# Kernel tuning notes

Measured on AMD Instinct MI355X. Metric: run time of the kernel, lower is better.

Reference implementation:

```python
import jax, jax.numpy as jnp
import numpy as np

K = 9          # kernel points along H (morph=0 -> kernel shape (9,1))
PAD = K // 2   # same padding along H
EPS = 1e-5     # batchnorm eps


def setup_inputs() -> dict:
    key = jax.random.key(0)
    ks = jax.random.split(key, 6)
    B, Cin, Cout, H, W = 4, 64, 64, 160, 160
    x = jax.random.normal(ks[0], (B, Cin, H, W), jnp.float32)
    # offset branch conv: 2*K offset channels, kernel (K,1)
    w_off = jax.random.normal(ks[1], (2 * K, Cin, K, 1), jnp.float32) * 0.05
    b_off = jax.random.normal(ks[2], (2 * K,), jnp.float32) * 0.05
    gamma = jnp.ones((2 * K,), jnp.float32)
    beta = jnp.zeros((2 * K,), jnp.float32)
    # deformable conv weights: kernel (K,1), groups=1
    w_def = jax.random.normal(ks[3], (Cout, Cin, K, 1), jnp.float32) * 0.05
    b_def = jax.random.normal(ks[4], (Cout,), jnp.float32) * 0.05
    return {"x": x, "w_off": w_off, "b_off": b_off, "gamma": gamma,
            "beta": beta, "w_def": w_def, "b_def": b_def}


def _convert_offsets(off):
    # morph=0: even channels (x) -> 0; odd channels (y) -> per-kernel-point cumsum
    c = K // 2
    y = off[:, 1::2]                                            # [B,K,H,W]
    top = jnp.flip(jnp.cumsum(jnp.flip(y[:, :c + 1], 1), 1), 1)  # suffix-cumsum to center
    bot = jnp.cumsum(jnp.concatenate([top[:, c:c + 1], y[:, c + 1:]], 1), 1)
    y_new = jnp.concatenate([top[:, :c], bot], 1)
    return jnp.zeros_like(off).at[:, 1::2].set(y_new)


def _deform_conv(x, off, w, b):
    B, C, H, W = x.shape
    dy = off[:, 0::2]                                           # [B,K,H,W]
    dx = off[:, 1::2]
    ky = jnp.arange(K, dtype=x.dtype).reshape(1, K, 1, 1)
    py = jnp.arange(H, dtype=x.dtype).reshape(1, 1, H, 1) - PAD + ky + dy
    px = jnp.arange(W, dtype=x.dtype).reshape(1, 1, 1, W) + dx
    y0 = jnp.floor(py)
    x0 = jnp.floor(px)
    fy = py - y0
    fx = px - x0
    y0i = y0.astype(jnp.int32)
    x0i = x0.astype(jnp.int32)
    xf = x.reshape(B, C, H * W)

    def gather(yc, xc):
        # zero-padded bilinear corner gather -> [B,C,K,H,W]
        valid = ((yc >= 0) & (yc < H) & (xc >= 0) & (xc < W)).astype(x.dtype)
        lin = jnp.clip(yc, 0, H - 1) * W + jnp.clip(xc, 0, W - 1)
        v = jax.vmap(lambda img, idx: img[:, idx])(xf, lin)
        return v * valid[:, None]

    w00 = ((1 - fy) * (1 - fx))[:, None]
    w01 = ((1 - fy) * fx)[:, None]
    w10 = (fy * (1 - fx))[:, None]
    w11 = (fy * fx)[:, None]
    samples = (w00 * gather(y0i, x0i) + w01 * gather(y0i, x0i + 1)
               + w10 * gather(y0i + 1, x0i) + w11 * gather(y0i + 1, x0i + 1))
    # contract kernel points and input channels
    return jnp.einsum('bckhw,ock->bohw', samples, w[:, :, :, 0]) + b[None, :, None, None]


def reference(x, w_off, b_off, gamma, beta, w_def, b_def):
    # offset branch: conv -> batchnorm (training-mode stats) -> tanh -> snake cumsum
    off = jax.lax.conv_general_dilated(
        x, w_off, (1, 1), ((PAD, PAD), (0, 0)),
        dimension_numbers=('NCHW', 'OIHW', 'NCHW')) + b_off[None, :, None, None]
    mu = off.mean((0, 2, 3), keepdims=True)
    var = off.var((0, 2, 3), keepdims=True)
    off = (off - mu) * jax.lax.rsqrt(var + EPS) * gamma[None, :, None, None] + beta[None, :, None, None]
    off = _convert_offsets(jnp.tanh(off))
    return _deform_conv(x, off, w_def, b_def)
```

## Files before the change

### kernel.cpp

```cpp
#include <hip/hip_runtime.h>
#include <hip/hip_fp16.h>
#include <math.h>

#define HW    25600
#define WID   160
#define HEI   160
#define BB    4
#define CIN   64
#define COUT  64
#define NBN   102400
#define TSTR  162

typedef _Float16 f16x8 __attribute__((ext_vector_type(8)));
typedef float    f32x4 __attribute__((ext_vector_type(4)));

union U4 { int i[4]; f16x8 v; };
union HU { unsigned u; __half2 h; };

__device__ __forceinline__ unsigned short f2h(float f) {
    return __half_as_ushort(__float2half(f));
}

__device__ __forceinline__ float ftanh(float x) {
    float e = __builtin_amdgcn_exp2f(x * 2.8853900817779268f);
    return 1.0f - 2.0f * __builtin_amdgcn_rcpf(e + 1.0f);
}

__global__ __launch_bounds__(256) void p0_prep(
        const float* __restrict__ x, const float* __restrict__ w_def,
        const float* __restrict__ w_off,
        unsigned short* __restrict__ xbT, unsigned short* __restrict__ wtA,
        unsigned short* __restrict__ wofA, float* __restrict__ stats) {
    int t = threadIdx.x;
    int blk = blockIdx.x;
    if (blk == 640) {
        for (int u = 0; u < 144; ++u) {
            int idx = t + u * 256;
            int k = idx >> 12;
            int r = idx & 4095;
            int chalf = r >> 11;
            int og = (r >> 9) & 3;
            int L = (r >> 3) & 63;
            int j = idx & 7;
            int o = og * 16 + (L & 15);
            int c = chalf * 32 + (L >> 4) * 8 + j;
            wtA[idx] = f2h(w_def[(o * CIN + c) * 9 + k]);
        }
        for (int u = 0; u < 36; ++u) {
            int idx = t + u * 256;
            int jj = idx & 7;
            int L  = (idx >> 3) & 63;
            int ch = (idx >> 9) & 1;
            int k  = idx >> 10;
            int j  = L & 15;
            int c  = ch * 32 + (L >> 4) * 8 + jj;
            wofA[idx] = (j < 9) ? f2h(w_off[((2 * j + 1) * CIN + c) * 9 + k])
                                : (unsigned short)0;
        }
        if (t < 32) stats[t] = 0.f;
        return;
    }
    __shared__ __align__(16) unsigned short tile[CIN * TSTR];
    int b = blk / HEI, h = blk % HEI;
    const float* xp = x + (b * CIN) * HW + h * WID;
    unsigned* ti = (unsigned*)tile;
#pragma unroll
    for (int u = 0; u < 10; ++u) {
        int e = t + u * 256;
        int c = e / 40, wq = e - c * 40;
        const float4 v = *(const float4*)(xp + c * HW + 4 * wq);
        unsigned p01 = f2h(v.x) | ((unsigned)f2h(v.y) << 16);
        unsigned p23 = f2h(v.z) | ((unsigned)f2h(v.w) << 16);
        ti[81 * c + 2 * wq]     = p01;
        ti[81 * c + 2 * wq + 1] = p23;
    }
    __syncthreads();
    unsigned* dst = (unsigned*)(xbT + (b * HEI + h) * (WID * 64));
#pragma unroll
    for (int u = 0; u < 20; ++u) {
        int e = t + u * 256;
        int w = e >> 5, cp = e & 31;
        unsigned lo = tile[(2 * cp) * TSTR + w];
        unsigned hi = tile[(2 * cp + 1) * TSTR + w];
        dst[e] = lo | (hi << 16);
    }
}

__global__ __launch_bounds__(320) void k1_offconv_mfma(
        const unsigned short* __restrict__ xbT,
        const unsigned short* __restrict__ wofA,
        const float* __restrict__ b_off,
        float* __restrict__ off_odd, float* __restrict__ stats) {
    int t = threadIdx.x;
    int blk = blockIdx.x;
    int xcd = blk & 7;
    int idx = blk >> 3;
    int b   = idx / 40;
    int r2  = idx - b * 40;
    int h   = xcd * 20 + (r2 >> 1);
    int p0  = (r2 & 1) * 80;
    int wave = t >> 6, lane = t & 63;
    int l15 = lane & 15, q = lane >> 4;
    int px  = p0 + wave * 16 + l15;

    f32x4 acc = (f32x4){0.f, 0.f, 0.f, 0.f};

    int klo = 4 - h;   if (klo < 0) klo = 0;
    int khi = 163 - h; if (khi > 8) khi = 8;

    for (int k = klo; k <= khi; ++k) {
        int py = h + k - 4;
        const unsigned short* sp = xbT + (b * HEI + py) * (WID * 64) + px * 64;
        f16x8 a0 = *(const f16x8*)(wofA + ((k * 2 + 0) * 64 + lane) * 8);
        f16x8 a1 = *(const f16x8*)(wofA + ((k * 2 + 1) * 64 + lane) * 8);
        f16x8 b0 = *(const f16x8*)(sp + q * 8);
        f16x8 b1 = *(const f16x8*)(sp + 32 + q * 8);
        acc = __builtin_amdgcn_mfma_f32_16x16x32_f16(a0, b0, acc, 0, 0, 0);
        acc = __builtin_amdgcn_mfma_f32_16x16x32_f16(a1, b1, acc, 0, 0, 0);
    }

    float sS[4] = {0.f, 0.f, 0.f, 0.f}, sQ[4] = {0.f, 0.f, 0.f, 0.f};
#pragma unroll
    for (int r = 0; r < 4; ++r) {
        int j = q * 4 + r;
        if (j < 9) {
            float v = acc[r] + b_off[2 * j + 1];
            off_odd[(b * 9 + j) * HW + h * WID + px] = v;
            sS[r] = v; sQ[r] = v * v;
        }
    }
#pragma unroll
    for (int o = 1; o < 16; o <<= 1) {
#pragma unroll
        for (int r = 0; r < 4; ++r) {
            sS[r] += __shfl_xor(sS[r], o);
            sQ[r] += __shfl_xor(sQ[r], o);
        }
    }
    __shared__ float redS[5][16], redQ[5][16];
    if (l15 == 0) {
#pragma unroll
        for (int r = 0; r < 4; ++r) {
            int j = q * 4 + r;
            if (j < 9) { redS[wave][j] = sS[r]; redQ[wave][j] = sQ[r]; }
        }
    }
    __syncthreads();
    if (t < 18) {
        int j = (t < 9) ? t : t - 9;
        float v = 0.f;
#pragma unroll
        for (int w = 0; w < 5; ++w)
            v += (t < 9) ? redS[w][j] : redQ[w][j];
        atomicAdd(&stats[t], v);
    }
}

__global__ __launch_bounds__(256, 5) void k4_deform_mfma(
        const unsigned short* __restrict__ xbT,
        const float* __restrict__ off_odd,
        const float* __restrict__ stats,
        const float* __restrict__ gamma,
        const float* __restrict__ beta,
        const unsigned short* __restrict__ wtA,
        const float* __restrict__ b_def,
        float* __restrict__ out) {
    __shared__ __align__(16) int S[2][80 * 36];
    __shared__ unsigned P0h[9][80], P1h[9][80];
    __shared__ int      PXI[9][80];

    int t   = threadIdx.x;
    int blk = blockIdx.x;
    int xcd = blk & 7;
    int idx = blk >> 3;
    int b   = idx / 40;
    int r2  = idx - b * 40;
    int h   = xcd * 20 + (r2 >> 1);
    int p0  = (r2 & 1) * 80;
    int wave = t >> 6, lane = t & 63;
    int l15 = lane & 15, q = lane >> 4;

    if (t < 80) {
        int px = p0 + t;
        float tv[9];
#pragma unroll
        for (int j = 0; j < 9; ++j) {
            float mean = stats[j] * (1.0f / NBN);
            float var  = stats[9 + j] * (1.0f / NBN) - mean * mean;
            float inv  = rsqrtf(var + 1e-5f);
            float v = off_odd[(b * 9 + j) * HW + h * WID + px];
            tv[j] = ftanh((v - mean) * inv * gamma[2 * j + 1] + beta[2 * j + 1]);
        }
        float dxv[9];
        dxv[4] = tv[4];
#pragma unroll
        for (int i = 5; i < 9; ++i) dxv[i] = dxv[i - 1] + tv[i];
#pragma unroll
        for (int i = 3; i >= 0; --i) dxv[i] = dxv[i + 1] + tv[i];
#pragma unroll
        for (int j = 0; j < 9; ++j) {
            int py = h + j - 4;
            bool rowok = (py >= 0) && (py < HEI);
            float pxf = (float)px + dxv[j];
            float x0f = floorf(pxf);
            float fx  = pxf - x0f;
            int   x0  = (int)x0f;
            float s0f = (rowok && x0 >= 0 && x0 < WID) ? 1.f - fx : 0.f;
            float s1f = (rowok && x0 >= -1 && x0 < WID - 1) ? fx : 0.f;
            unsigned h0 = f2h(s0f), h1 = f2h(s1f);
            P0h[j][t] = h0 | (h0 << 16);
            P1h[j][t] = h1 | (h1 << 16);
            int xi0 = min(max(x0, 0), WID - 1);
            int xi1 = min(max(x0 + 1, 0), WID - 1);
            PXI[j][t] = xi0 | (xi1 << 16);
        }
    }
    __syncthreads();

    f32x4 acc[5];
#pragma unroll
    for (int i = 0; i < 5; ++i) acc[i] = (f32x4){0.f, 0.f, 0.f, 0.f};

    int4     A4[3], B4[3];
    unsigned sa[3], sb[3];
    f16x8    wpa, wpb;

#define PF(kk)                                                                  \
    {                                                                           \
        int pyc = min(max(h + (kk) - 4, 0), HEI - 1);                           \
        const int4* rowI4 = (const int4*)(xbT + (b * HEI + pyc) * (WID * 64));  \
        _Pragma("unroll")                                                       \
        for (int u = 0; u < 3; ++u) {                                           \
            if (u < 2 || t < 128) {                                             \
                int id = t + u * 256;                                           \
                int pxl = id >> 3, c4 = id & 7;                                 \
                int xi = PXI[kk][pxl];                                          \
                sa[u] = P0h[kk][pxl];                                           \
                sb[u] = P1h[kk][pxl];                                           \
                A4[u] = rowI4[(xi & 0xffff) * 8 + c4];                          \
                B4[u] = rowI4[(xi >> 16) * 8 + c4];                             \
            }                                                                   \
        }                                                                       \
        wpa = *(const f16x8*)(wtA + ((((kk) * 2 + 0) * 4 + wave) * 64 + lane) * 8); \
        wpb = *(const f16x8*)(wtA + ((((kk) * 2 + 1) * 4 + wave) * 64 + lane) * 8); \
    }

    PF(0);
    int buf = 0;

    for (int k = 0; k < 9; ++k) {
        int* Sb = S[buf];
#pragma unroll
        for (int u = 0; u < 3; ++u) {
            if (u < 2 || t < 128) {
                int id = t + u * 256;
                int pxl = id >> 3, c4 = id & 7;
                HU sah, sbh; sah.u = sa[u]; sbh.u = sb[u];
                int4 r4;
                HU a, bb, r;
#pragma unroll
                for (int ii = 0; ii < 4; ++ii) {
                    a.u  = (unsigned)(&A4[u].x)[ii];
                    bb.u = (unsigned)(&B4[u].x)[ii];
                    r.h  = __hfma2(sbh.h, bb.h, __hmul2(sah.h, a.h));
                    (&r4.x)[ii] = (int)r.u;
                }
                *(int4*)(Sb + pxl * 36 + (c4 << 2)) = r4;
            }
        }
        __syncthreads();

        f16x8 wf0 = wpa, wf1 = wpb;
        if (k < 8) PF(k + 1);

#pragma unroll
        for (int pxt = 0; pxt < 5; ++pxt) {
            const int* sp = &Sb[(pxt * 16 + l15) * 36];
            U4 u0, u1;
            *(int4*)u0.i = *(const int4*)(sp + q * 4);
            *(int4*)u1.i = *(const int4*)(sp + 16 + q * 4);
            acc[pxt] = __builtin_amdgcn_mfma_f32_16x16x32_f16(wf0, u0.v, acc[pxt], 0, 0, 0);
            acc[pxt] = __builtin_amdgcn_mfma_f32_16x16x32_f16(wf1, u1.v, acc[pxt], 0, 0, 0);
        }
        buf ^= 1;
    }
#undef PF

    float bd[4];
#pragma unroll
    for (int r = 0; r < 4; ++r) bd[r] = b_def[wave * 16 + q * 4 + r];
#pragma unroll
    for (int pxt = 0; pxt < 5; ++pxt) {
#pragma unroll
        for (int r = 0; r < 4; ++r) {
            int o = wave * 16 + q * 4 + r;
            out[(b * COUT + o) * HW + h * WID + p0 + pxt * 16 + l15] = acc[pxt][r] + bd[r];
        }
    }
}

extern "C" void kernel_launch(void* const* d_in, const int* in_sizes, int n_in,
                              void* d_out, int out_size, void* d_ws, size_t ws_size,
                              hipStream_t stream) {
    const float* x     = (const float*)d_in[0];
    const float* w_off = (const float*)d_in[1];
    const float* b_off = (const float*)d_in[2];
    const float* gamma = (const float*)d_in[3];
    const float* beta  = (const float*)d_in[4];
    const float* w_def = (const float*)d_in[5];
    const float* b_def = (const float*)d_in[6];
    float* out = (float*)d_out;

    float* off_odd       = (float*)d_ws;
    float* stats         = off_odd + 921600;
    unsigned short* wtA  = (unsigned short*)(stats + 32);
    unsigned short* wofA = wtA + 36864;
    unsigned short* xbT  = wofA + 9216;

    p0_prep<<<641, 256, 0, stream>>>(x, w_def, w_off, xbT, wtA, wofA, stats);
    k1_offconv_mfma<<<1280, 320, 0, stream>>>(xbT, wofA, b_off, off_odd, stats);
    k4_deform_mfma<<<1280, 256, 0, stream>>>(xbT, off_odd, stats, gamma, beta,
                                             wtA, b_def, out);
}
```

Before: 154.2 us.

## Spread weight prep over blocks, unroll offset conv with zero row, shard stats atomics

Measured after the change: 130.4 us. -15.4%, faster.

```diff
diff --git a/kernel.cpp b/kernel.cpp
--- a/kernel.cpp
+++ b/kernel.cpp
@@ -10,6 +10,7 @@
 #define COUT  64
 #define NBN   102400
 #define TSTR  162
+#define ZROW  640
 
 typedef _Float16 f16x8 __attribute__((ext_vector_type(8)));
 typedef float    f32x4 __attribute__((ext_vector_type(4)));
@@ -33,9 +34,11 @@
         unsigned short* __restrict__ wofA, float* __restrict__ stats) {
     int t = threadIdx.x;
     int blk = blockIdx.x;
-    if (blk == 640) {
-        for (int u = 0; u < 144; ++u) {
-            int idx = t + u * 256;
+    if (blk >= 640) {
+        int wb = blk - 640;
+#pragma unroll
+        for (int u = 0; u < 18; ++u) {
+            int idx = t + (wb * 18 + u) * 256;
             int k = idx >> 12;
             int r = idx & 4095;
             int chalf = r >> 11;
@@ -46,18 +49,26 @@
             int c = chalf * 32 + (L >> 4) * 8 + j;
             wtA[idx] = f2h(w_def[(o * CIN + c) * 9 + k]);
         }
-        for (int u = 0; u < 36; ++u) {
-            int idx = t + u * 256;
-            int jj = idx & 7;
-            int L  = (idx >> 3) & 63;
-            int ch = (idx >> 9) & 1;
-            int k  = idx >> 10;
-            int j  = L & 15;
-            int c  = ch * 32 + (L >> 4) * 8 + jj;
-            wofA[idx] = (j < 9) ? f2h(w_off[((2 * j + 1) * CIN + c) * 9 + k])
-                                : (unsigned short)0;
-        }
-        if (t < 32) stats[t] = 0.f;
+        if (wb < 4) {
+#pragma unroll
+            for (int u = 0; u < 9; ++u) {
+                int idx = t + (wb * 9 + u) * 256;
+                int jj = idx & 7;
+                int L  = (idx >> 3) & 63;
+                int ch = (idx >> 9) & 1;
+                int k  = idx >> 10;
+                int j  = L & 15;
+                int c  = ch * 32 + (L >> 4) * 8 + jj;
+                wofA[idx] = (j < 9) ? f2h(w_off[((2 * j + 1) * CIN + c) * 9 + k])
+                                    : (unsigned short)0;
+            }
+        } else {
+            unsigned* z = (unsigned*)(xbT + ZROW * (WID * 64));
+#pragma unroll
+            for (int u = 0; u < 5; ++u)
+                z[((wb - 4) * 5 + u) * 256 + t] = 0;
+        }
+        if (wb == 0) stats[t] = 0.f;
         return;
     }
     __shared__ __align__(16) unsigned short tile[CIN * TSTR];
@@ -103,20 +114,23 @@
     int l15 = lane & 15, q = lane >> 4;
     int px  = p0 + wave * 16 + l15;
 
+    f16x8 wa[9], wb[9];
+#pragma unroll
+    for (int k = 0; k < 9; ++k) {
+        wa[k] = *(const f16x8*)(wofA + ((k * 2 + 0) * 64 + lane) * 8);
+        wb[k] = *(const f16x8*)(wofA + ((k * 2 + 1) * 64 + lane) * 8);
+    }
+
     f32x4 acc = (f32x4){0.f, 0.f, 0.f, 0.f};
-
-    int klo = 4 - h;   if (klo < 0) klo = 0;
-    int khi = 163 - h; if (khi > 8) khi = 8;
-
-    for (int k = klo; k <= khi; ++k) {
-        int py = h + k - 4;
-        const unsigned short* sp = xbT + (b * HEI + py) * (WID * 64) + px * 64;
-        f16x8 a0 = *(const f16x8*)(wofA + ((k * 2 + 0) * 64 + lane) * 8);
-        f16x8 a1 = *(const f16x8*)(wofA + ((k * 2 + 1) * 64 + lane) * 8);
+#pragma unroll
+    for (int k = 0; k < 9; ++k) {
+        int py  = h + k - 4;
+        int row = ((unsigned)py < HEI) ? (b * HEI + py) : ZROW;
+        const unsigned short* sp = xbT + row * (WID * 64) + px * 64;
         f16x8 b0 = *(const f16x8*)(sp + q * 8);
         f16x8 b1 = *(const f16x8*)(sp + 32 + q * 8);
-        acc = __builtin_amdgcn_mfma_f32_16x16x32_f16(a0, b0, acc, 0, 0, 0);
-        acc = __builtin_amdgcn_mfma_f32_16x16x32_f16(a1, b1, acc, 0, 0, 0);
+        acc = __builtin_amdgcn_mfma_f32_16x16x32_f16(wa[k], b0, acc, 0, 0, 0);
+        acc = __builtin_amdgcn_mfma_f32_16x16x32_f16(wb[k], b1, acc, 0, 0, 0);
     }
 
     float sS[4] = {0.f, 0.f, 0.f, 0.f}, sQ[4] = {0.f, 0.f, 0.f, 0.f};
@@ -152,7 +166,7 @@
 #pragma unroll
         for (int w = 0; w < 5; ++w)
             v += (t < 9) ? redS[w][j] : redQ[w][j];
-        atomicAdd(&stats[t], v);
+        atomicAdd(&stats[xcd * 32 + t], v);
     }
 }
 
@@ -168,6 +182,7 @@
     __shared__ __align__(16) int S[2][80 * 36];
     __shared__ unsigned P0h[9][80], P1h[9][80];
     __shared__ int      PXI[9][80];
+    __shared__ float    ssum[18];
 
     int t   = threadIdx.x;
     int blk = blockIdx.x;
@@ -180,39 +195,56 @@
     int wave = t >> 6, lane = t & 63;
     int l15 = lane & 15, q = lane >> 4;
 
-    if (t < 80) {
-        int px = p0 + t;
-        float tv[9];
-#pragma unroll
-        for (int j = 0; j < 9; ++j) {
-            float mean = stats[j] * (1.0f / NBN);
-            float var  = stats[9 + j] * (1.0f / NBN) - mean * mean;
+    if (t < 18) {
+        float v = 0.f;
+#pragma unroll
+        for (int xx = 0; xx < 8; ++xx) v += stats[xx * 32 + t];
+        ssum[t] = v;
+    }
+    __syncthreads();
+
+    if (t < 160) {
+        int half = (t >= 80) ? 1 : 0;
+        int pxl  = t - half * 80;
+        int px   = p0 + pxl;
+        int j0   = half * 4;
+        float tv[5];
+#pragma unroll
+        for (int u = 0; u < 5; ++u) {
+            int j = j0 + u;
+            float mean = ssum[j] * (1.0f / NBN);
+            float var  = ssum[9 + j] * (1.0f / NBN) - mean * mean;
             float inv  = rsqrtf(var + 1e-5f);
             float v = off_odd[(b * 9 + j) * HW + h * WID + px];
-            tv[j] = ftanh((v - mean) * inv * gamma[2 * j + 1] + beta[2 * j + 1]);
-        }
-        float dxv[9];
-        dxv[4] = tv[4];
-#pragma unroll
-        for (int i = 5; i < 9; ++i) dxv[i] = dxv[i - 1] + tv[i];
-#pragma unroll
-        for (int i = 3; i >= 0; --i) dxv[i] = dxv[i + 1] + tv[i];
-#pragma unroll
-        for (int j = 0; j < 9; ++j) {
+            tv[u] = ftanh((v - mean) * inv * gamma[2 * j + 1] + beta[2 * j + 1]);
+        }
+        float dxv[5];
+        if (half == 0) {
+            dxv[4] = tv[4];
+#pragma unroll
+            for (int i = 3; i >= 0; --i) dxv[i] = dxv[i + 1] + tv[i];
+        } else {
+            dxv[0] = tv[0];
+#pragma unroll
+            for (int i = 1; i < 5; ++i) dxv[i] = dxv[i - 1] + tv[i];
+        }
+#pragma unroll
+        for (int u = 0; u < 5; ++u) {
+            int j = j0 + u;
             int py = h + j - 4;
             bool rowok = (py >= 0) && (py < HEI);
-            float pxf = (float)px + dxv[j];
+            float pxf = (float)px + dxv[u];
             float x0f = floorf(pxf);
             float fx  = pxf - x0f;
             int   x0  = (int)x0f;
             float s0f = (rowok && x0 >= 0 && x0 < WID) ? 1.f - fx : 0.f;
             float s1f = (rowok && x0 >= -1 && x0 < WID - 1) ? fx : 0.f;
             unsigned h0 = f2h(s0f), h1 = f2h(s1f);
-            P0h[j][t] = h0 | (h0 << 16);
-            P1h[j][t] = h1 | (h1 << 16);
+            P0h[j][pxl] = h0 | (h0 << 16);
+            P1h[j][pxl] = h1 | (h1 << 16);
             int xi0 = min(max(x0, 0), WID - 1);
             int xi1 = min(max(x0 + 1, 0), WID - 1);
-            PXI[j][t] = xi0 | (xi1 << 16);
+            PXI[j][pxl] = xi0 | (xi1 << 16);
         }
     }
     __syncthreads();
@@ -313,11 +345,11 @@
 
     float* off_odd       = (float*)d_ws;
     float* stats         = off_odd + 921600;
-    unsigned short* wtA  = (unsigned short*)(stats + 32);
+    unsigned short* wtA  = (unsigned short*)(stats + 256);
     unsigned short* wofA = wtA + 36864;
     unsigned short* xbT  = wofA + 9216;
 
-    p0_prep<<<641, 256, 0, stream>>>(x, w_def, w_off, xbT, wtA, wofA, stats);
+    p0_prep<<<648, 256, 0, stream>>>(x, w_def, w_off, xbT, wtA, wofA, stats);
     k1_offconv_mfma<<<1280, 320, 0, stream>>>(xbT, wofA, b_off, off_odd, stats);
     k4_deform_mfma<<<1280, 256, 0, stream>>>(xbT, off_odd, stats, gamma, beta,
                                              wtA, b_def, out);
```
